# Optimization experiments

Hardware: AMD Instinct MI355X
Metric: run time of the kernel (lower is better)

## Reference

```python
import jax, jax.numpy as jnp
import numpy as np

N = 100000      # num_nodes
E = 3200000     # num_edges (avg degree 32)
DIN, DH, DOUT = 128, 128, 64
S, L = 3, 3     # num_scales, num_layers
EPS = 1e-5


def setup_inputs() -> dict:
    key = jax.random.key(0)
    ks = jax.random.split(key, 12)
    sc = 0.05
    x = jax.random.normal(ks[0], (N, DIN), jnp.float32)
    edge_index = jax.random.randint(ks[1], (2, E), 0, N, jnp.int32)
    return {
        'x': x,
        'edge_index': edge_index,
        'W0': jax.random.normal(ks[2], (S, DIN, DH), jnp.float32) * sc,
        'b0': jnp.zeros((S, DH), jnp.float32),
        'W1': jax.random.normal(ks[3], (S, DH, DH), jnp.float32) * sc,
        'b1': jnp.zeros((S, DH), jnp.float32),
        'W2': jax.random.normal(ks[4], (S, DH, DOUT), jnp.float32) * sc,
        'b2': jnp.zeros((S, DOUT), jnp.float32),
        'gamma': jnp.ones((S * L, DH), jnp.float32),   # layer_norms (only first L-1 per scale used)
        'beta': jnp.zeros((S * L, DH), jnp.float32),
        'Wf': jax.random.normal(ks[5], (S * DOUT, DOUT), jnp.float32) * sc,
        'bf': jnp.zeros((DOUT,), jnp.float32),
    }


def _layer_norm(h, g, b):
    mu = jnp.mean(h, axis=-1, keepdims=True)
    var = jnp.mean(jnp.square(h - mu), axis=-1, keepdims=True)
    return (h - mu) * jax.lax.rsqrt(var + EPS) * g + b


def _gcn(h, W, b, src, dst, dis):
    # GCNConv: D^{-1/2}(A+I)D^{-1/2} h W + b  (self-loops handled separately)
    hw = h @ W
    msg = hw[src] * (dis[src] * dis[dst])[:, None]          # gather + edge-scale
    agg = jax.ops.segment_sum(msg, dst, num_segments=N)     # scatter-add
    agg = agg + hw * (dis * dis)[:, None]                   # self-loop term
    return agg + b


def reference(x, edge_index, W0, b0, W1, b1, W2, b2, gamma, beta, Wf, bf):
    src, dst = edge_index[0], edge_index[1]
    # degree on A + I (unit edge weights + self loop)
    deg = jax.ops.segment_sum(jnp.ones((E,), x.dtype), dst, num_segments=N) + 1.0
    dis = jax.lax.rsqrt(deg)

    scale_outputs = []
    for s in range(S):
        h = _gcn(x, W0[s], b0[s], src, dst, dis)
        h = _layer_norm(jax.nn.relu(h), gamma[s * L + 0], beta[s * L + 0])  # dropout=identity (eval)
        h = _gcn(h, W1[s], b1[s], src, dst, dis)
        h = _layer_norm(jax.nn.relu(h), gamma[s * L + 1], beta[s * L + 1])
        h = _gcn(h, W2[s], b2[s], src, dst, dis)
        scale_outputs.append(h)

    fused = jnp.concatenate(scale_outputs, axis=-1)  # [N, S*DOUT]
    return fused @ Wf + bf
```

## Files before the change

kernel.cpp:

```cpp
#include <hip/hip_runtime.h>

#define DIN 128
#define DH 128
#define DOUTC 64
#define NS 3
#define NL 3
#define EPSV 1e-5f

typedef __attribute__((ext_vector_type(8))) short bf16x8;
typedef __attribute__((ext_vector_type(4))) float f32x4;

static __device__ inline float bf2f(unsigned short h) {
    unsigned int u = ((unsigned int)h) << 16;
    return __builtin_bit_cast(float, u);
}
static __device__ inline unsigned short f2bf(float f) {
    unsigned int u = __builtin_bit_cast(unsigned int, f);
    u += 0x7fffu + ((u >> 16) & 1u);
    return (unsigned short)(u >> 16);
}
static __device__ inline float lo16(unsigned int u) {
    return __builtin_bit_cast(float, u << 16);
}
static __device__ inline float hi16(unsigned int u) {
    return __builtin_bit_cast(float, u & 0xffff0000u);
}
static __device__ inline unsigned int pkbf(float lo, float hi) {
    return ((unsigned int)f2bf(hi) << 16) | f2bf(lo);
}
static __device__ inline float sext8(unsigned int u, int k) {
    return (float)((int)(u << (24 - 8 * k)) >> 24);
}
static __device__ inline unsigned int pk8(float a, float b, float c, float d, float qs) {
    int q0 = (int)rintf(a * qs), q1 = (int)rintf(b * qs);
    int q2 = (int)rintf(c * qs), q3 = (int)rintf(d * qs);
    return (q0 & 255) | ((q1 & 255) << 8) | ((q2 & 255) << 16) | ((q3 & 255) << 24);
}

__global__ __launch_bounds__(256) void k_count_r(const int* __restrict__ dst,
                                                 int* __restrict__ counts, int e, int n) {
    int rg = blockIdx.x & 7;
    int lo = rg * (n >> 3);
    int hi = (rg == 7) ? n : lo + (n >> 3);
    int nb = gridDim.x >> 3, bi = blockIdx.x >> 3;
    int e4 = e >> 2;
    const int4* dst4 = (const int4*)dst;
    for (int i = bi * 256 + threadIdx.x; i < e4; i += nb * 256) {
        int4 d = dst4[i];
        if (d.x >= lo && d.x < hi) atomicAdd(&counts[d.x], 1);
        if (d.y >= lo && d.y < hi) atomicAdd(&counts[d.y], 1);
        if (d.z >= lo && d.z < hi) atomicAdd(&counts[d.z], 1);
        if (d.w >= lo && d.w < hi) atomicAdd(&counts[d.w], 1);
    }
    if (bi == 0 && (int)threadIdx.x < (e & 3)) {
        int d = dst[e4 * 4 + threadIdx.x];
        if (d >= lo && d < hi) atomicAdd(&counts[d], 1);
    }
}

__global__ void k_dis(const int* __restrict__ counts, float* __restrict__ dis, int n) {
    int i = blockIdx.x * blockDim.x + threadIdx.x;
    if (i < n) dis[i] = rsqrtf((float)counts[i] + 1.0f);
}

__global__ void k_scanA(const int* __restrict__ counts, int* __restrict__ row_start,
                        int* __restrict__ bsums, int n) {
    __shared__ int s[512];
    int t = threadIdx.x;
    int i = blockIdx.x * 512 + t;
    int v = (i < n) ? counts[i] : 0;
    s[t] = v;
    __syncthreads();
    for (int off = 1; off < 512; off <<= 1) {
        int x = s[t];
        if (t >= off) x += s[t - off];
        __syncthreads();
        s[t] = x;
        __syncthreads();
    }
    if (i < n) row_start[i] = s[t] - v;
    if (t == 511) bsums[blockIdx.x] = s[511];
}

__global__ void k_scanB(int* __restrict__ bsums, int nb) {
    __shared__ int s[256];
    int t = threadIdx.x;
    int v = (t < nb) ? bsums[t] : 0;
    s[t] = v;
    __syncthreads();
    for (int off = 1; off < 256; off <<= 1) {
        int x = s[t];
        if (t >= off) x += s[t - off];
        __syncthreads();
        s[t] = x;
        __syncthreads();
    }
    if (t < nb) bsums[t] = s[t] - v;
}

__global__ void k_scanC(int* __restrict__ row_start, const int* __restrict__ bsums, int n) {
    int i = blockIdx.x * blockDim.x + threadIdx.x;
    if (i < n) row_start[i] += bsums[i >> 9];
}

__global__ __launch_bounds__(256) void k_fill_r(const int* __restrict__ src,
                                                const int* __restrict__ dst,
                                                int* __restrict__ cursor,
                                                int* __restrict__ col, int e, int n) {
    int rg = blockIdx.x & 7;
    int lo = rg * (n >> 3);
    int hi = (rg == 7) ? n : lo + (n >> 3);
    int nb = gridDim.x >> 3, bi = blockIdx.x >> 3;
    int e4 = e >> 2;
    const int4* dst4 = (const int4*)dst;
    const int4* src4 = (const int4*)src;
    for (int i = bi * 256 + threadIdx.x; i < e4; i += nb * 256) {
        int4 d = dst4[i];
        int4 s = src4[i];
        if (d.x >= lo && d.x < hi) col[atomicAdd(&cursor[d.x], 1)] = s.x;
        if (d.y >= lo && d.y < hi) col[atomicAdd(&cursor[d.y], 1)] = s.y;
        if (d.z >= lo && d.z < hi) col[atomicAdd(&cursor[d.z], 1)] = s.z;
        if (d.w >= lo && d.w < hi) col[atomicAdd(&cursor[d.w], 1)] = s.w;
    }
    if (bi == 0 && (int)threadIdx.x < (e & 3)) {
        int d = dst[e4 * 4 + threadIdx.x];
        int s = src[e4 * 4 + threadIdx.x];
        if (d >= lo && d < hi) col[atomicAdd(&cursor[d], 1)] = s;
    }
}

__global__ void k_prep_w(const float* __restrict__ W0, const float* __restrict__ W1,
                         const float* __restrict__ W2, const float* __restrict__ Wf,
                         const float* __restrict__ b2, const float* __restrict__ bf,
                         unsigned short* __restrict__ Wt0hi, unsigned short* __restrict__ Wt0lo,
                         unsigned short* __restrict__ Wt1hi, unsigned short* __restrict__ Wt1lo,
                         unsigned short* __restrict__ Mhi, unsigned short* __restrict__ Mlo,
                         float* __restrict__ bcomb) {
    int idx = blockIdx.x * blockDim.x + threadIdx.x;
    if (idx < NS * DH * DH) {
        int s = idx / (DH * DH);
        int rem = idx % (DH * DH);
        int o = rem / DH, i = rem % DH;
        {
            float v = W0[(size_t)s * DH * DH + (size_t)i * DH + o];
            unsigned short h = f2bf(v);
            Wt0hi[idx] = h;
            Wt0lo[idx] = f2bf(v - bf2f(h));
        }
        {
            float v = W1[(size_t)s * DH * DH + (size_t)i * DH + o];
            unsigned short h = f2bf(v);
            Wt1hi[idx] = h;
            Wt1lo[idx] = f2bf(v - bf2f(h));
        }
    }
    if (idx < DOUTC * NS * DH) {
        int o = idx / (NS * DH);
        int k = idx % (NS * DH);
        int s = k / DH, i = k % DH;
        float acc = 0.f;
        for (int c = 0; c < DOUTC; ++c)
            acc += W2[((size_t)s * DH + i) * DOUTC + c] * Wf[((size_t)s * DOUTC + c) * DOUTC + o];
        unsigned short h = f2bf(acc);
        Mhi[idx] = h;
        Mlo[idx] = f2bf(acc - bf2f(h));
    }
    if (idx < DOUTC) {
        float acc = bf[idx];
        for (int s = 0; s < NS; ++s)
            for (int c = 0; c < DOUTC; ++c)
                acc += b2[s * DOUTC + c] * Wf[((size_t)s * DOUTC + c) * DOUTC + idx];
        bcomb[idx] = acc;
    }
}

__global__ __launch_bounds__(256) void k_cvtq(const float2* __restrict__ x,
                                              unsigned int* __restrict__ xq,
                                              float* __restrict__ xs,
                                              const float* __restrict__ dis, int n) {
    int wid = ((blockIdx.x * blockDim.x + threadIdx.x) >> 6);
    int lane = threadIdx.x & 63;
    if (wid >= n) return;
    float2 v = x[(size_t)wid * 64 + lane];
    float m = fmaxf(fabsf(v.x), fabsf(v.y));
    #pragma unroll
    for (int off = 32; off; off >>= 1) m = fmaxf(m, __shfl_xor(m, off));
    float qs = m > 0.f ? 127.f / m : 0.f;
    int q0 = (int)rintf(v.x * qs), q1 = (int)rintf(v.y * qs);
    ((unsigned short*)xq)[(size_t)wid * 64 + lane] =
        (unsigned short)((q0 & 255) | ((q1 & 255) << 8));
    if (lane == 0) xs[wid] = dis[wid] * m * (1.f / 127.f);
}

__global__ __launch_bounds__(256) void k_quant384(const unsigned int* __restrict__ h,
                                                  unsigned int* __restrict__ hq,
                                                  float* __restrict__ hs, int n) {
    int wid = ((blockIdx.x * blockDim.x + threadIdx.x) >> 6);
    int lane = threadIdx.x & 63;
    int half = lane >> 5, c = lane & 31;
    int v = wid * 2 + half;
    if (v >= n) return;
    const uint2* p = (const uint2*)(h + (size_t)v * 192);
    uint2 w0 = p[c], w1 = p[c + 32], w2 = p[c + 64];
    float f[12] = {lo16(w0.x), hi16(w0.x), lo16(w0.y), hi16(w0.y),
                   lo16(w1.x), hi16(w1.x), lo16(w1.y), hi16(w1.y),
                   lo16(w2.x), hi16(w2.x), lo16(w2.y), hi16(w2.y)};
    float m = 0.f;
    #pragma unroll
    for (int k = 0; k < 12; ++k) m = fmaxf(m, fabsf(f[k]));
    #pragma unroll
    for (int off = 16; off; off >>= 1) m = fmaxf(m, __shfl_xor(m, off));
    float qs = m > 0.f ? 127.f / m : 0.f;
    unsigned int* po = hq + (size_t)v * 96;
    po[c]      = pk8(f[0], f[1], f[2], f[3], qs);
    po[c + 32] = pk8(f[4], f[5], f[6], f[7], qs);
    po[c + 64] = pk8(f[8], f[9], f[10], f[11], qs);
    if (c == 0) hs[v] = m * (1.f / 127.f);
}

__global__ __launch_bounds__(256) void k_quant64(const unsigned int* __restrict__ qb,
                                                 unsigned int* __restrict__ qq,
                                                 float* __restrict__ qs2, int n) {
    int wid = ((blockIdx.x * blockDim.x + threadIdx.x) >> 6);
    int lane = threadIdx.x & 63;
    int g = lane >> 4, c = lane & 15;
    int v = wid * 4 + g;
    if (v >= n) return;
    uint2 w = ((const uint2*)(qb + (size_t)v * 32))[c];
    float f0 = lo16(w.x), f1 = hi16(w.x), f2 = lo16(w.y), f3 = hi16(w.y);
    float m = fmaxf(fmaxf(fabsf(f0), fabsf(f1)), fmaxf(fabsf(f2), fabsf(f3)));
    #pragma unroll
    for (int off = 8; off; off >>= 1) m = fmaxf(m, __shfl_xor(m, off));
    float qs = m > 0.f ? 127.f / m : 0.f;
    qq[(size_t)v * 16 + c] = pk8(f0, f1, f2, f3, qs);
    if (c == 0) qs2[v] = m * (1.f / 127.f);
}

__global__ __launch_bounds__(256) void k_agg128q(
        const unsigned int* __restrict__ xq, const float* __restrict__ xs,
        unsigned int* __restrict__ z0, const float* __restrict__ dis,
        const int* __restrict__ rowstart, const int* __restrict__ counts,
        const int* __restrict__ col, int n) {
    int wid = (blockIdx.x * blockDim.x + threadIdx.x) >> 6;
    int lane = threadIdx.x & 63;
    int half = lane >> 5, c = lane & 31;
    int nw = (gridDim.x * blockDim.x) >> 6;
    int ntask = (n + 1) >> 1;
    for (int w = wid; w < ntask; w += nw) {
        int v = w * 2 + half;
        int vc = v < n ? v : n - 1;
        float dv = dis[vc];
        const int* colp = col + rowstart[vc];
        int cnt = v < n ? counts[vc] : 0;
        unsigned int us = xq[(size_t)vc * 32 + c];
        float sv = xs[vc];
        float a0 = sv * sext8(us, 0), a1 = sv * sext8(us, 1);
        float a2 = sv * sext8(us, 2), a3 = sv * sext8(us, 3);
        int i = 0;
        for (; i + 8 <= cnt; i += 8) {
            #pragma unroll
            for (int k = 0; k < 8; ++k) {
                int s0 = colp[i + k];
                float sc = xs[s0];
                unsigned int u = xq[(size_t)s0 * 32 + c];
                a0 += sc * sext8(u, 0); a1 += sc * sext8(u, 1);
                a2 += sc * sext8(u, 2); a3 += sc * sext8(u, 3);
            }
        }
        for (; i < cnt; ++i) {
            int s0 = colp[i];
            float sc = xs[s0];
            unsigned int u = xq[(size_t)s0 * 32 + c];
            a0 += sc * sext8(u, 0); a1 += sc * sext8(u, 1);
            a2 += sc * sext8(u, 2); a3 += sc * sext8(u, 3);
        }
        if (v < n) {
            uint2 o = {pkbf(dv * a0, dv * a1), pkbf(dv * a2, dv * a3)};
            *(uint2*)&z0[(size_t)v * 64 + 2 * c] = o;
        }
    }
}

__global__ __launch_bounds__(256) void k_agg384q(
        const unsigned int* __restrict__ hq, const float* __restrict__ hs,
        unsigned int* __restrict__ g1, const float* __restrict__ dis,
        const int* __restrict__ rowstart, const int* __restrict__ counts,
        const int* __restrict__ col, int n) {
    int wid = (blockIdx.x * blockDim.x + threadIdx.x) >> 6;
    int lane = threadIdx.x & 63;
    int half = lane >> 5, c = lane & 31;
    int nw = (gridDim.x * blockDim.x) >> 6;
    int ntask = (n + 1) >> 1;
    for (int w = wid; w < ntask; w += nw) {
        int v = w * 2 + half;
        int vc = v < n ? v : n - 1;
        float dv = dis[vc];
        const int* colp = col + rowstart[vc];
        int cnt = v < n ? counts[vc] : 0;
        const unsigned int* rp = hq + (size_t)vc * 96;
        unsigned int u0 = rp[c], u1 = rp[c + 32], u2 = rp[c + 64];
        float sv = hs[vc];
        float a[12];
        #pragma unroll
        for (int k = 0; k < 4; ++k) {
            a[k]     = sv * sext8(u0, k);
            a[4 + k] = sv * sext8(u1, k);
            a[8 + k] = sv * sext8(u2, k);
        }
        int i = 0;
        for (; i + 4 <= cnt; i += 4) {
            #pragma unroll
            for (int k4 = 0; k4 < 4; ++k4) {
                int s0 = colp[i + k4];
                float sc = hs[s0];
                const unsigned int* p0 = hq + (size_t)s0 * 96;
                unsigned int w0 = p0[c], w1 = p0[c + 32], w2 = p0[c + 64];
                #pragma unroll
                for (int k = 0; k < 4; ++k) {
                    a[k]     += sc * sext8(w0, k);
                    a[4 + k] += sc * sext8(w1, k);
                    a[8 + k] += sc * sext8(w2, k);
                }
            }
        }
        for (; i < cnt; ++i) {
            int s0 = colp[i];
            float sc = hs[s0];
            const unsigned int* p0 = hq + (size_t)s0 * 96;
            unsigned int w0 = p0[c], w1 = p0[c + 32], w2 = p0[c + 64];
            #pragma unroll
            for (int k = 0; k < 4; ++k) {
                a[k]     += sc * sext8(w0, k);
                a[4 + k] += sc * sext8(w1, k);
                a[8 + k] += sc * sext8(w2, k);
            }
        }
        if (v < n) {
            unsigned int* po = g1 + (size_t)v * 192;
            uint2 o0 = {pkbf(dv * a[0], dv * a[1]), pkbf(dv * a[2], dv * a[3])};
            *(uint2*)&po[2 * c] = o0;
            uint2 o1 = {pkbf(dv * a[4], dv * a[5]), pkbf(dv * a[6], dv * a[7])};
            *(uint2*)&po[2 * c + 64] = o1;
            uint2 o2 = {pkbf(dv * a[8], dv * a[9]), pkbf(dv * a[10], dv * a[11])};
            *(uint2*)&po[2 * c + 128] = o2;
        }
    }
}

__global__ __launch_bounds__(256) void k_agg64q(
        const unsigned int* __restrict__ qq, const float* __restrict__ qs2,
        float* __restrict__ out, const float* __restrict__ bcomb,
        const float* __restrict__ dis, const int* __restrict__ rowstart,
        const int* __restrict__ counts, const int* __restrict__ col, int n) {
    int wid = (blockIdx.x * blockDim.x + threadIdx.x) >> 6;
    int lane = threadIdx.x & 63;
    int g = lane >> 4, c = lane & 15;
    int nw = (gridDim.x * blockDim.x) >> 6;
    int ntask = (n + 3) >> 2;
    float4 bc = ((const float4*)bcomb)[c];
    for (int w = wid; w < ntask; w += nw) {
        int v = w * 4 + g;
        int vc = v < n ? v : n - 1;
        float dv = dis[vc];
        const int* colp = col + rowstart[vc];
        int cnt = v < n ? counts[vc] : 0;
        unsigned int us = qq[(size_t)vc * 16 + c];
        float sv = qs2[vc];
        float a0 = sv * sext8(us, 0), a1 = sv * sext8(us, 1);
        float a2 = sv * sext8(us, 2), a3 = sv * sext8(us, 3);
        int i = 0;
        for (; i + 8 <= cnt; i += 8) {
            #pragma unroll
            for (int k = 0; k < 8; ++k) {
                int s0 = colp[i + k];
                float sc = qs2[s0];
                unsigned int u = qq[(size_t)s0 * 16 + c];
                a0 += sc * sext8(u, 0); a1 += sc * sext8(u, 1);
                a2 += sc * sext8(u, 2); a3 += sc * sext8(u, 3);
            }
        }
        for (; i < cnt; ++i) {
            int s0 = colp[i];
            float sc = qs2[s0];
            unsigned int u = qq[(size_t)s0 * 16 + c];
            a0 += sc * sext8(u, 0); a1 += sc * sext8(u, 1);
            a2 += sc * sext8(u, 2); a3 += sc * sext8(u, 3);
        }
        if (v < n) {
            float4 o = make_float4(dv * a0 + bc.x, dv * a1 + bc.y,
                                   dv * a2 + bc.z, dv * a3 + bc.w);
            *(float4*)&out[(size_t)v * 64 + 4 * c] = o;
        }
    }
}

__global__ __launch_bounds__(256) void k_gemm0(
        const unsigned short* __restrict__ A, const unsigned short* __restrict__ Whi,
        const unsigned short* __restrict__ Wlo, const float* __restrict__ bias,
        const float* __restrict__ gamma, const float* __restrict__ beta,
        const float* __restrict__ dis, unsigned short* __restrict__ out, int n) {
    int wave = threadIdx.x >> 6, lane = threadIdx.x & 63;
    int g = blockIdx.x * 4 + wave;
    if (g * 16 >= n) return;
    int r16 = lane & 15, g4 = lane >> 4;
    int row = g * 16 + r16;
    if (row >= n) row = n - 1;

    bf16x8 a[4];
    #pragma unroll
    for (int ks = 0; ks < 4; ++ks)
        a[ks] = *(const bf16x8*)&A[(size_t)row * DH + ks * 32 + g4 * 8];

    for (int s = 0; s < NS; ++s) {
        const unsigned short* whi = Whi + (size_t)s * DH * DH;
        const unsigned short* wlo = Wlo + (size_t)s * DH * DH;
        f32x4 acc[8];
        #pragma unroll
        for (int t = 0; t < 8; ++t) acc[t] = (f32x4){0.f, 0.f, 0.f, 0.f};
        #pragma unroll
        for (int ks = 0; ks < 4; ++ks) {
            #pragma unroll
            for (int t = 0; t < 8; ++t) {
                size_t wofs = (size_t)(t * 16 + r16) * DH + ks * 32 + g4 * 8;
                bf16x8 bh = *(const bf16x8*)&whi[wofs];
                bf16x8 bl = *(const bf16x8*)&wlo[wofs];
                acc[t] = __builtin_amdgcn_mfma_f32_16x16x32_bf16(a[ks], bh, acc[t], 0, 0, 0);
                acc[t] = __builtin_amdgcn_mfma_f32_16x16x32_bf16(a[ks], bl, acc[t], 0, 0, 0);
            }
        }
        float bia[8], gam[8], bet[8];
        #pragma unroll
        for (int t = 0; t < 8; ++t) {
            bia[t] = bias[s * DH + t * 16 + r16];
            gam[t] = gamma[(size_t)(s * NL + 0) * DH + t * 16 + r16];
            bet[t] = beta[(size_t)(s * NL + 0) * DH + t * 16 + r16];
        }
        #pragma unroll
        for (int r = 0; r < 4; ++r) {
            float y[8];
            float sm = 0.f, q = 0.f;
            #pragma unroll
            for (int t = 0; t < 8; ++t) {
                y[t] = fmaxf(acc[t][r] + bia[t], 0.f);
                sm += y[t];
                q += y[t] * y[t];
            }
            #pragma unroll
            for (int off = 8; off; off >>= 1) {
                sm += __shfl_xor(sm, off);
                q += __shfl_xor(q, off);
            }
            float mu = sm * (1.f / 128.f);
            float var = q * (1.f / 128.f) - mu * mu;
            float rstd = rsqrtf(var + EPSV);
            int node = g * 16 + g4 * 4 + r;
            if (node < n) {
                float dnode = dis[node];
                #pragma unroll
                for (int t = 0; t < 8; ++t) {
                    float o = ((y[t] - mu) * rstd * gam[t] + bet[t]) * dnode;
                    out[(size_t)node * (NS * DH) + s * DH + t * 16 + r16] = f2bf(o);
                }
            }
        }
    }
}

__global__ __launch_bounds__(256) void k_gemm1q(
        const unsigned short* __restrict__ G, const unsigned short* __restrict__ Whi,
        const unsigned short* __restrict__ Wlo, const unsigned short* __restrict__ Mhi,
        const unsigned short* __restrict__ Mlo, const float* __restrict__ bias,
        const float* __restrict__ gamma, const float* __restrict__ beta,
        const float* __restrict__ dis, unsigned short* __restrict__ q, int n) {
    __shared__ __align__(16) unsigned short sH[4][16][392];
    int wave = threadIdx.x >> 6, lane = threadIdx.x & 63;
    int g = blockIdx.x * 4 + wave;
    if (g * 16 >= n) return;
    int r16 = lane & 15, g4 = lane >> 4;
    int row = g * 16 + r16;
    if (row >= n) row = n - 1;

    for (int s = 0; s < NS; ++s) {
        bf16x8 a[4];
        #pragma unroll
        for (int ks = 0; ks < 4; ++ks)
            a[ks] = *(const bf16x8*)&G[(size_t)row * (NS * DH) + s * DH + ks * 32 + g4 * 8];
        const unsigned short* whi = Whi + (size_t)s * DH * DH;
        const unsigned short* wlo = Wlo + (size_t)s * DH * DH;
        f32x4 acc[8];
        #pragma unroll
        for (int t = 0; t < 8; ++t) acc[t] = (f32x4){0.f, 0.f, 0.f, 0.f};
        #pragma unroll
        for (int ks = 0; ks < 4; ++ks) {
            #pragma unroll
            for (int t = 0; t < 8; ++t) {
                size_t wofs = (size_t)(t * 16 + r16) * DH + ks * 32 + g4 * 8;
                bf16x8 bh = *(const bf16x8*)&whi[wofs];
                bf16x8 bl = *(const bf16x8*)&wlo[wofs];
                acc[t] = __builtin_amdgcn_mfma_f32_16x16x32_bf16(a[ks], bh, acc[t], 0, 0, 0);
                acc[t] = __builtin_amdgcn_mfma_f32_16x16x32_bf16(a[ks], bl, acc[t], 0, 0, 0);
            }
        }
        float bia[8], gam[8], bet[8];
        #pragma unroll
        for (int t = 0; t < 8; ++t) {
            bia[t] = bias[s * DH + t * 16 + r16];
            gam[t] = gamma[(size_t)(s * NL + 1) * DH + t * 16 + r16];
            bet[t] = beta[(size_t)(s * NL + 1) * DH + t * 16 + r16];
        }
        #pragma unroll
        for (int r = 0; r < 4; ++r) {
            float y[8];
            float sm = 0.f, qq = 0.f;
            #pragma unroll
            for (int t = 0; t < 8; ++t) {
                y[t] = fmaxf(acc[t][r] + bia[t], 0.f);
                sm += y[t];
                qq += y[t] * y[t];
            }
            #pragma unroll
            for (int off = 8; off; off >>= 1) {
                sm += __shfl_xor(sm, off);
                qq += __shfl_xor(qq, off);
            }
            float mu = sm * (1.f / 128.f);
            float var = qq * (1.f / 128.f) - mu * mu;
            float rstd = rsqrtf(var + EPSV);
            #pragma unroll
            for (int t = 0; t < 8; ++t) {
                float o = (y[t] - mu) * rstd * gam[t] + bet[t];
                sH[wave][g4 * 4 + r][s * DH + t * 16 + r16] = f2bf(o);
            }
        }
    }
    __syncthreads();
    f32x4 qa[4];
    #pragma unroll
    for (int t = 0; t < 4; ++t) qa[t] = (f32x4){0.f, 0.f, 0.f, 0.f};
    #pragma unroll
    for (int ks = 0; ks < 12; ++ks) {
        bf16x8 av = *(const bf16x8*)&sH[wave][r16][ks * 32 + g4 * 8];
        #pragma unroll
        for (int t = 0; t < 4; ++t) {
            size_t wofs = (size_t)(t * 16 + r16) * (NS * DH) + ks * 32 + g4 * 8;
            bf16x8 bh = *(const bf16x8*)&Mhi[wofs];
            bf16x8 bl = *(const bf16x8*)&Mlo[wofs];
            qa[t] = __builtin_amdgcn_mfma_f32_16x16x32_bf16(av, bh, qa[t], 0, 0, 0);
            qa[t] = __builtin_amdgcn_mfma_f32_16x16x32_bf16(av, bl, qa[t], 0, 0, 0);
        }
    }
    #pragma unroll
    for (int r = 0; r < 4; ++r) {
        int node = g * 16 + g4 * 4 + r;
        if (node < n) {
            float dnode = dis[node];
            #pragma unroll
            for (int t = 0; t < 4; ++t)
                q[(size_t)node * DOUTC + t * 16 + r16] = f2bf(qa[t][r] * dnode);
        }
    }
}

extern "C" void kernel_launch(void* const* d_in, const int* in_sizes, int n_in,
                              void* d_out, int out_size, void* d_ws, size_t ws_size,
                              hipStream_t stream) {
    const float* x    = (const float*)d_in[0];
    const int*   ei   = (const int*)d_in[1];
    const float* W0   = (const float*)d_in[2];
    const float* b0   = (const float*)d_in[3];
    const float* W1   = (const float*)d_in[4];
    const float* b1   = (const float*)d_in[5];
    const float* W2   = (const float*)d_in[6];
    const float* b2   = (const float*)d_in[7];
    const float* gamma= (const float*)d_in[8];
    const float* beta = (const float*)d_in[9];
    const float* Wf   = (const float*)d_in[10];
    const float* bf   = (const float*)d_in[11];
    float* out = (float*)d_out;

    const int n = in_sizes[0] / DIN;
    const int e = in_sizes[1] / 2;
    const int* src = ei;
    const int* dst = ei + e;

    char* ws = (char*)d_ws;
    auto alloc = [&](size_t bytes) {
        char* p = ws;
        ws += (bytes + 255) & ~(size_t)255;
        return p;
    };
    int*   counts   = (int*)alloc((size_t)n * 4);
    int*   cursor   = (int*)alloc((size_t)n * 4);
    int*   rowstart = (int*)alloc((size_t)n * 4);
    int*   bsums    = (int*)alloc(4096);
    float* dis      = (float*)alloc((size_t)n * 4);
    int*   col      = (int*)alloc((size_t)e * 4);
    unsigned short* Wt0hi = (unsigned short*)alloc((size_t)NS * DH * DH * 2);
    unsigned short* Wt0lo = (unsigned short*)alloc((size_t)NS * DH * DH * 2);
    unsigned short* Wt1hi = (unsigned short*)alloc((size_t)NS * DH * DH * 2);
    unsigned short* Wt1lo = (unsigned short*)alloc((size_t)NS * DH * DH * 2);
    unsigned short* Mhi   = (unsigned short*)alloc((size_t)DOUTC * NS * DH * 2);
    unsigned short* Mlo   = (unsigned short*)alloc((size_t)DOUTC * NS * DH * 2);
    float* bcomb    = (float*)alloc(DOUTC * 4);
    unsigned int* xq  = (unsigned int*)alloc((size_t)n * 32 * 4);
    float* xs         = (float*)alloc((size_t)n * 4);
    unsigned short* z0    = (unsigned short*)alloc((size_t)n * DH * 2);
    unsigned short* h1cat = (unsigned short*)alloc((size_t)n * NS * DH * 2);
    unsigned int* h1q = (unsigned int*)alloc((size_t)n * 96 * 4);
    float* hs         = (float*)alloc((size_t)n * 4);
    unsigned short* g1cat = (unsigned short*)alloc((size_t)n * NS * DH * 2);
    unsigned short* q     = (unsigned short*)alloc((size_t)n * DOUTC * 2);
    unsigned int* qq  = (unsigned int*)alloc((size_t)n * 16 * 4);
    float* qs2        = (float*)alloc((size_t)n * 4);

    hipMemsetAsync(counts, 0, (size_t)n * 4, stream);

    k_count_r<<<2048, 256, 0, stream>>>(dst, counts, e, n);
    k_dis<<<(n + 255) / 256, 256, 0, stream>>>(counts, dis, n);

    int nb = (n + 511) / 512;
    k_scanA<<<nb, 512, 0, stream>>>(counts, rowstart, bsums, n);
    k_scanB<<<1, 256, 0, stream>>>(bsums, nb);
    k_scanC<<<(n + 255) / 256, 256, 0, stream>>>(rowstart, bsums, n);
    hipMemcpyAsync(cursor, rowstart, (size_t)n * 4, hipMemcpyDeviceToDevice, stream);
    k_fill_r<<<2048, 256, 0, stream>>>(src, dst, cursor, col, e, n);

    k_prep_w<<<(NS * DH * DH + 255) / 256, 256, 0, stream>>>(
        W0, W1, W2, Wf, b2, bf, Wt0hi, Wt0lo, Wt1hi, Wt1lo, Mhi, Mlo, bcomb);
    k_cvtq<<<(n + 3) / 4, 256, 0, stream>>>((const float2*)x, xq, xs, dis, n);

    k_agg128q<<<2048, 256, 0, stream>>>(xq, xs, (unsigned int*)z0,
                                        dis, rowstart, counts, col, n);
    const int GG = (n / 16 + 3) / 4;
    k_gemm0<<<GG, 256, 0, stream>>>(z0, Wt0hi, Wt0lo, b0, gamma, beta, dis, h1cat, n);
    k_quant384<<<(n + 7) / 8, 256, 0, stream>>>((const unsigned int*)h1cat, h1q, hs, n);
    k_agg384q<<<2048, 256, 0, stream>>>(h1q, hs, (unsigned int*)g1cat,
                                        dis, rowstart, counts, col, n);
    k_gemm1q<<<GG, 256, 0, stream>>>(g1cat, Wt1hi, Wt1lo, Mhi, Mlo,
                                     b1, gamma, beta, dis, q, n);
    k_quant64<<<(n + 15) / 16, 256, 0, stream>>>((const unsigned int*)q, qq, qs2, n);
    k_agg64q<<<2048, 256, 0, stream>>>(qq, qs2, out, bcomb,
                                       dis, rowstart, counts, col, n);
}
```

Before: 1.242 ms.

## Fuse int8 quantization into GEMM epilogues with permuted channel layout

Layer-0 GEMM now quantizes its LayerNorm output straight to int8 with a per-scale scale factor, removing the separate quant384 kernel and the bf16 h1cat round trip. Channels are stored in a permuted order so each lane writes contiguous packed words, and W1 and the fused W2·Wf matrix are permuted to match. The second GEMM is split into k_gemm1, which writes bf16 h2, and k_gemmq, which does the final projection and quantizes inline, replacing gemm1q's shared-memory staging and the quant64 kernel. The trade-off is an extra global write and read of h2 and three per-scale quantization scales instead of one.

```diff
diff --git a/kernel.cpp b/kernel.cpp
--- a/kernel.cpp
+++ b/kernel.cpp
@@ -148,7 +148,10 @@
             Wt0lo[idx] = f2bf(v - bf2f(h));
         }
         {
-            float v = W1[(size_t)s * DH * DH + (size_t)i * DH + o];
+            int lp = i;
+            int p = lp >> 6, r = (lp >> 2) & 15, k = lp & 3;
+            int lchan = (4 * p + k) * 16 + r;
+            float v = W1[(size_t)s * DH * DH + (size_t)lchan * DH + o];
             unsigned short h = f2bf(v);
             Wt1hi[idx] = h;
             Wt1lo[idx] = f2bf(v - bf2f(h));
@@ -156,11 +159,13 @@
     }
     if (idx < DOUTC * NS * DH) {
         int o = idx / (NS * DH);
-        int k = idx % (NS * DH);
-        int s = k / DH, i = k % DH;
+        int pos = idx % (NS * DH);
+        int s = pos >> 7, lp = pos & 127;
+        int p = lp >> 6, r = (lp >> 2) & 15, k = lp & 3;
+        int il = (4 * p + k) * 16 + r;
         float acc = 0.f;
         for (int c = 0; c < DOUTC; ++c)
-            acc += W2[((size_t)s * DH + i) * DOUTC + c] * Wf[((size_t)s * DOUTC + c) * DOUTC + o];
+            acc += W2[((size_t)s * DH + il) * DOUTC + c] * Wf[((size_t)s * DOUTC + c) * DOUTC + o];
         unsigned short h = f2bf(acc);
         Mhi[idx] = h;
         Mlo[idx] = f2bf(acc - bf2f(h));
@@ -190,50 +195,6 @@
     ((unsigned short*)xq)[(size_t)wid * 64 + lane] =
         (unsigned short)((q0 & 255) | ((q1 & 255) << 8));
     if (lane == 0) xs[wid] = dis[wid] * m * (1.f / 127.f);
-}
-
-__global__ __launch_bounds__(256) void k_quant384(const unsigned int* __restrict__ h,
-                                                  unsigned int* __restrict__ hq,
-                                                  float* __restrict__ hs, int n) {
-    int wid = ((blockIdx.x * blockDim.x + threadIdx.x) >> 6);
-    int lane = threadIdx.x & 63;
-    int half = lane >> 5, c = lane & 31;
-    int v = wid * 2 + half;
-    if (v >= n) return;
-    const uint2* p = (const uint2*)(h + (size_t)v * 192);
-    uint2 w0 = p[c], w1 = p[c + 32], w2 = p[c + 64];
-    float f[12] = {lo16(w0.x), hi16(w0.x), lo16(w0.y), hi16(w0.y),
-                   lo16(w1.x), hi16(w1.x), lo16(w1.y), hi16(w1.y),
-                   lo16(w2.x), hi16(w2.x), lo16(w2.y), hi16(w2.y)};
-    float m = 0.f;
-    #pragma unroll
-    for (int k = 0; k < 12; ++k) m = fmaxf(m, fabsf(f[k]));
-    #pragma unroll
-    for (int off = 16; off; off >>= 1) m = fmaxf(m, __shfl_xor(m, off));
-    float qs = m > 0.f ? 127.f / m : 0.f;
-    unsigned int* po = hq + (size_t)v * 96;
-    po[c]      = pk8(f[0], f[1], f[2], f[3], qs);
-    po[c + 32] = pk8(f[4], f[5], f[6], f[7], qs);
-    po[c + 64] = pk8(f[8], f[9], f[10], f[11], qs);
-    if (c == 0) hs[v] = m * (1.f / 127.f);
-}
-
-__global__ __launch_bounds__(256) void k_quant64(const unsigned int* __restrict__ qb,
-                                                 unsigned int* __restrict__ qq,
-                                                 float* __restrict__ qs2, int n) {
-    int wid = ((blockIdx.x * blockDim.x + threadIdx.x) >> 6);
-    int lane = threadIdx.x & 63;
-    int g = lane >> 4, c = lane & 15;
-    int v = wid * 4 + g;
-    if (v >= n) return;
-    uint2 w = ((const uint2*)(qb + (size_t)v * 32))[c];
-    float f0 = lo16(w.x), f1 = hi16(w.x), f2 = lo16(w.y), f3 = hi16(w.y);
-    float m = fmaxf(fmaxf(fabsf(f0), fabsf(f1)), fmaxf(fabsf(f2), fabsf(f3)));
-    #pragma unroll
-    for (int off = 8; off; off >>= 1) m = fmaxf(m, __shfl_xor(m, off));
-    float qs = m > 0.f ? 127.f / m : 0.f;
-    qq[(size_t)v * 16 + c] = pk8(f0, f1, f2, f3, qs);
-    if (c == 0) qs2[v] = m * (1.f / 127.f);
 }
 
 __global__ __launch_bounds__(256) void k_agg128q(
@@ -281,8 +242,89 @@
     }
 }
 
-__global__ __launch_bounds__(256) void k_agg384q(
-        const unsigned int* __restrict__ hq, const float* __restrict__ hs,
+__global__ __launch_bounds__(256, 4) void k_gemm0i(
+        const unsigned short* __restrict__ A, const unsigned short* __restrict__ Whi,
+        const unsigned short* __restrict__ Wlo, const float* __restrict__ bias,
+        const float* __restrict__ gamma, const float* __restrict__ beta,
+        const float* __restrict__ dis, unsigned int* __restrict__ h1q,
+        float* __restrict__ hs4, int n) {
+    int wave = threadIdx.x >> 6, lane = threadIdx.x & 63;
+    int g = blockIdx.x * 4 + wave;
+    if (g * 16 >= n) return;
+    int r16 = lane & 15, g4 = lane >> 4;
+    int row = g * 16 + r16;
+    if (row >= n) row = n - 1;
+
+    bf16x8 a[4];
+    #pragma unroll
+    for (int ks = 0; ks < 4; ++ks)
+        a[ks] = *(const bf16x8*)&A[(size_t)row * DH + ks * 32 + g4 * 8];
+
+    for (int s = 0; s < NS; ++s) {
+        const unsigned short* whi = Whi + (size_t)s * DH * DH;
+        const unsigned short* wlo = Wlo + (size_t)s * DH * DH;
+        f32x4 acc[8];
+        #pragma unroll
+        for (int t = 0; t < 8; ++t) acc[t] = (f32x4){0.f, 0.f, 0.f, 0.f};
+        #pragma unroll
+        for (int ks = 0; ks < 4; ++ks) {
+            #pragma unroll
+            for (int t = 0; t < 8; ++t) {
+                size_t wofs = (size_t)(t * 16 + r16) * DH + ks * 32 + g4 * 8;
+                bf16x8 bh = *(const bf16x8*)&whi[wofs];
+                bf16x8 bl = *(const bf16x8*)&wlo[wofs];
+                acc[t] = __builtin_amdgcn_mfma_f32_16x16x32_bf16(a[ks], bh, acc[t], 0, 0, 0);
+                acc[t] = __builtin_amdgcn_mfma_f32_16x16x32_bf16(a[ks], bl, acc[t], 0, 0, 0);
+            }
+        }
+        float bia[8], gam[8], bet[8];
+        #pragma unroll
+        for (int t = 0; t < 8; ++t) {
+            bia[t] = bias[s * DH + t * 16 + r16];
+            gam[t] = gamma[(size_t)(s * NL + 0) * DH + t * 16 + r16];
+            bet[t] = beta[(size_t)(s * NL + 0) * DH + t * 16 + r16];
+        }
+        #pragma unroll
+        for (int r = 0; r < 4; ++r) {
+            float y[8];
+            float sm = 0.f, q = 0.f;
+            #pragma unroll
+            for (int t = 0; t < 8; ++t) {
+                y[t] = fmaxf(acc[t][r] + bia[t], 0.f);
+                sm += y[t];
+                q += y[t] * y[t];
+            }
+            #pragma unroll
+            for (int off = 8; off; off >>= 1) {
+                sm += __shfl_xor(sm, off);
+                q += __shfl_xor(q, off);
+            }
+            float mu = sm * (1.f / 128.f);
+            float var = q * (1.f / 128.f) - mu * mu;
+            float rstd = rsqrtf(var + EPSV);
+            float o[8];
+            float m = 0.f;
+            #pragma unroll
+            for (int t = 0; t < 8; ++t) {
+                o[t] = (y[t] - mu) * rstd * gam[t] + bet[t];
+                m = fmaxf(m, fabsf(o[t]));
+            }
+            #pragma unroll
+            for (int off = 8; off; off >>= 1) m = fmaxf(m, __shfl_xor(m, off));
+            float qs = m > 0.f ? 127.f / m : 0.f;
+            int node = g * 16 + g4 * 4 + r;
+            if (node < n) {
+                unsigned int* pn = h1q + (size_t)node * 96;
+                pn[(s * 2 + 0) * 16 + r16] = pk8(o[0], o[1], o[2], o[3], qs);
+                pn[(s * 2 + 1) * 16 + r16] = pk8(o[4], o[5], o[6], o[7], qs);
+                if (r16 == 0) hs4[(size_t)node * 4 + s] = dis[node] * m * (1.f / 127.f);
+            }
+        }
+    }
+}
+
+__global__ __launch_bounds__(256) void k_agg384qp(
+        const unsigned int* __restrict__ hq, const float* __restrict__ hs4,
         unsigned int* __restrict__ g1, const float* __restrict__ dis,
         const int* __restrict__ rowstart, const int* __restrict__ counts,
         const int* __restrict__ col, int n) {
@@ -299,50 +341,166 @@
         int cnt = v < n ? counts[vc] : 0;
         const unsigned int* rp = hq + (size_t)vc * 96;
         unsigned int u0 = rp[c], u1 = rp[c + 32], u2 = rp[c + 64];
-        float sv = hs[vc];
+        float4 sv = ((const float4*)hs4)[vc];
         float a[12];
         #pragma unroll
         for (int k = 0; k < 4; ++k) {
-            a[k]     = sv * sext8(u0, k);
-            a[4 + k] = sv * sext8(u1, k);
-            a[8 + k] = sv * sext8(u2, k);
+            a[k]     = sv.x * sext8(u0, k);
+            a[4 + k] = sv.y * sext8(u1, k);
+            a[8 + k] = sv.z * sext8(u2, k);
         }
         int i = 0;
         for (; i + 4 <= cnt; i += 4) {
             #pragma unroll
             for (int k4 = 0; k4 < 4; ++k4) {
                 int s0 = colp[i + k4];
-                float sc = hs[s0];
+                float4 sc = ((const float4*)hs4)[s0];
                 const unsigned int* p0 = hq + (size_t)s0 * 96;
                 unsigned int w0 = p0[c], w1 = p0[c + 32], w2 = p0[c + 64];
                 #pragma unroll
                 for (int k = 0; k < 4; ++k) {
-                    a[k]     += sc * sext8(w0, k);
-                    a[4 + k] += sc * sext8(w1, k);
-                    a[8 + k] += sc * sext8(w2, k);
+                    a[k]     += sc.x * sext8(w0, k);
+                    a[4 + k] += sc.y * sext8(w1, k);
+                    a[8 + k] += sc.z * sext8(w2, k);
                 }
             }
         }
         for (; i < cnt; ++i) {
             int s0 = colp[i];
-            float sc = hs[s0];
+            float4 sc = ((const float4*)hs4)[s0];
             const unsigned int* p0 = hq + (size_t)s0 * 96;
             unsigned int w0 = p0[c], w1 = p0[c + 32], w2 = p0[c + 64];
             #pragma unroll
             for (int k = 0; k < 4; ++k) {
-                a[k]     += sc * sext8(w0, k);
-                a[4 + k] += sc * sext8(w1, k);
-                a[8 + k] += sc * sext8(w2, k);
+                a[k]     += sc.x * sext8(w0, k);
+                a[4 + k] += sc.y * sext8(w1, k);
+                a[8 + k] += sc.z * sext8(w2, k);
             }
         }
         if (v < n) {
             unsigned int* po = g1 + (size_t)v * 192;
+            int b = ((c >> 4) & 1) * 32 + (c & 15) * 2;
             uint2 o0 = {pkbf(dv * a[0], dv * a[1]), pkbf(dv * a[2], dv * a[3])};
-            *(uint2*)&po[2 * c] = o0;
+            *(uint2*)&po[b] = o0;
             uint2 o1 = {pkbf(dv * a[4], dv * a[5]), pkbf(dv * a[6], dv * a[7])};
-            *(uint2*)&po[2 * c + 64] = o1;
+            *(uint2*)&po[b + 64] = o1;
             uint2 o2 = {pkbf(dv * a[8], dv * a[9]), pkbf(dv * a[10], dv * a[11])};
-            *(uint2*)&po[2 * c + 128] = o2;
+            *(uint2*)&po[b + 128] = o2;
+        }
+    }
+}
+
+__global__ __launch_bounds__(256, 4) void k_gemm1(
+        const unsigned short* __restrict__ G, const unsigned short* __restrict__ Whi,
+        const unsigned short* __restrict__ Wlo, const float* __restrict__ bias,
+        const float* __restrict__ gamma, const float* __restrict__ beta,
+        unsigned int* __restrict__ h2, int n) {
+    int wave = threadIdx.x >> 6, lane = threadIdx.x & 63;
+    int g = blockIdx.x * 4 + wave;
+    if (g * 16 >= n) return;
+    int r16 = lane & 15, g4 = lane >> 4;
+    int row = g * 16 + r16;
+    if (row >= n) row = n - 1;
+
+    for (int s = 0; s < NS; ++s) {
+        bf16x8 a[4];
+        #pragma unroll
+        for (int ks = 0; ks < 4; ++ks)
+            a[ks] = *(const bf16x8*)&G[(size_t)row * (NS * DH) + s * DH + ks * 32 + g4 * 8];
+        const unsigned short* whi = Whi + (size_t)s * DH * DH;
+        const unsigned short* wlo = Wlo + (size_t)s * DH * DH;
+        f32x4 acc[8];
+        #pragma unroll
+        for (int t = 0; t < 8; ++t) acc[t] = (f32x4){0.f, 0.f, 0.f, 0.f};
+        #pragma unroll
+        for (int ks = 0; ks < 4; ++ks) {
+            #pragma unroll
+            for (int t = 0; t < 8; ++t) {
+                size_t wofs = (size_t)(t * 16 + r16) * DH + ks * 32 + g4 * 8;
+                bf16x8 bh = *(const bf16x8*)&whi[wofs];
+                bf16x8 bl = *(const bf16x8*)&wlo[wofs];
+                acc[t] = __builtin_amdgcn_mfma_f32_16x16x32_bf16(a[ks], bh, acc[t], 0, 0, 0);
+                acc[t] = __builtin_amdgcn_mfma_f32_16x16x32_bf16(a[ks], bl, acc[t], 0, 0, 0);
+            }
+        }
+        float bia[8], gam[8], bet[8];
+        #pragma unroll
+        for (int t = 0; t < 8; ++t) {
+            bia[t] = bias[s * DH + t * 16 + r16];
+            gam[t] = gamma[(size_t)(s * NL + 1) * DH + t * 16 + r16];
+            bet[t] = beta[(size_t)(s * NL + 1) * DH + t * 16 + r16];
+        }
+        #pragma unroll
+        for (int r = 0; r < 4; ++r) {
+            float y[8];
+            float sm = 0.f, qq = 0.f;
+            #pragma unroll
+            for (int t = 0; t < 8; ++t) {
+                y[t] = fmaxf(acc[t][r] + bia[t], 0.f);
+                sm += y[t];
+                qq += y[t] * y[t];
+            }
+            #pragma unroll
+            for (int off = 8; off; off >>= 1) {
+                sm += __shfl_xor(sm, off);
+                qq += __shfl_xor(qq, off);
+            }
+            float mu = sm * (1.f / 128.f);
+            float var = qq * (1.f / 128.f) - mu * mu;
+            float rstd = rsqrtf(var + EPSV);
+            float o[8];
+            #pragma unroll
+            for (int t = 0; t < 8; ++t)
+                o[t] = (y[t] - mu) * rstd * gam[t] + bet[t];
+            int node = g * 16 + g4 * 4 + r;
+            if (node < n) {
+                unsigned int* po = h2 + (size_t)node * 192;
+                uint2 w0 = {pkbf(o[0], o[1]), pkbf(o[2], o[3])};
+                *(uint2*)&po[s * 64 + r16 * 2] = w0;
+                uint2 w1 = {pkbf(o[4], o[5]), pkbf(o[6], o[7])};
+                *(uint2*)&po[s * 64 + 32 + r16 * 2] = w1;
+            }
+        }
+    }
+}
+
+__global__ __launch_bounds__(256, 4) void k_gemmq(
+        const unsigned short* __restrict__ H, const unsigned short* __restrict__ Mhi,
+        const unsigned short* __restrict__ Mlo, const float* __restrict__ dis,
+        unsigned int* __restrict__ qq, float* __restrict__ qs2, int n) {
+    int wave = threadIdx.x >> 6, lane = threadIdx.x & 63;
+    int g = blockIdx.x * 4 + wave;
+    if (g * 16 >= n) return;
+    int r16 = lane & 15, g4 = lane >> 4;
+    int row = g * 16 + r16;
+    if (row >= n) row = n - 1;
+
+    f32x4 qa[4];
+    #pragma unroll
+    for (int t = 0; t < 4; ++t) qa[t] = (f32x4){0.f, 0.f, 0.f, 0.f};
+    #pragma unroll
+    for (int ks = 0; ks < 12; ++ks) {
+        bf16x8 av = *(const bf16x8*)&H[(size_t)row * (NS * DH) + ks * 32 + g4 * 8];
+        #pragma unroll
+        for (int t = 0; t < 4; ++t) {
+            size_t wofs = (size_t)(t * 16 + r16) * (NS * DH) + ks * 32 + g4 * 8;
+            bf16x8 bh = *(const bf16x8*)&Mhi[wofs];
+            bf16x8 bl = *(const bf16x8*)&Mlo[wofs];
+            qa[t] = __builtin_amdgcn_mfma_f32_16x16x32_bf16(av, bh, qa[t], 0, 0, 0);
+            qa[t] = __builtin_amdgcn_mfma_f32_16x16x32_bf16(av, bl, qa[t], 0, 0, 0);
+        }
+    }
+    #pragma unroll
+    for (int r = 0; r < 4; ++r) {
+        float v0 = qa[0][r], v1 = qa[1][r], v2 = qa[2][r], v3 = qa[3][r];
+        float m = fmaxf(fmaxf(fabsf(v0), fabsf(v1)), fmaxf(fabsf(v2), fabsf(v3)));
+        #pragma unroll
+        for (int off = 8; off; off >>= 1) m = fmaxf(m, __shfl_xor(m, off));
+        float qs = m > 0.f ? 127.f / m : 0.f;
+        int node = g * 16 + g4 * 4 + r;
+        if (node < n) {
+            qq[(size_t)node * 16 + r16] = pk8(v0, v1, v2, v3, qs);
+            if (r16 == 0) qs2[node] = dis[node] * m * (1.f / 127.f);
         }
     }
 }
@@ -357,7 +515,7 @@
     int g = lane >> 4, c = lane & 15;
     int nw = (gridDim.x * blockDim.x) >> 6;
     int ntask = (n + 3) >> 2;
-    float4 bc = ((const float4*)bcomb)[c];
+    float bc0 = bcomb[c], bc1 = bcomb[16 + c], bc2 = bcomb[32 + c], bc3 = bcomb[48 + c];
     for (int w = wid; w < ntask; w += nw) {
         int v = w * 4 + g;
         int vc = v < n ? v : n - 1;
@@ -387,176 +545,11 @@
             a2 += sc * sext8(u, 2); a3 += sc * sext8(u, 3);
         }
         if (v < n) {
-            float4 o = make_float4(dv * a0 + bc.x, dv * a1 + bc.y,
-                                   dv * a2 + bc.z, dv * a3 + bc.w);
-            *(float4*)&out[(size_t)v * 64 + 4 * c] = o;
-        }
-    }
-}
-
-__global__ __launch_bounds__(256) void k_gemm0(
-        const unsigned short* __restrict__ A, const unsigned short* __restrict__ Whi,
-        const unsigned short* __restrict__ Wlo, const float* __restrict__ bias,
-        const float* __restrict__ gamma, const float* __restrict__ beta,
-        const float* __restrict__ dis, unsigned short* __restrict__ out, int n) {
-    int wave = threadIdx.x >> 6, lane = threadIdx.x & 63;
-    int g = blockIdx.x * 4 + wave;
-    if (g * 16 >= n) return;
-    int r16 = lane & 15, g4 = lane >> 4;
-    int row = g * 16 + r16;
-    if (row >= n) row = n - 1;
-
-    bf16x8 a[4];
-    #pragma unroll
-    for (int ks = 0; ks < 4; ++ks)
-        a[ks] = *(const bf16x8*)&A[(size_t)row * DH + ks * 32 + g4 * 8];
-
-    for (int s = 0; s < NS; ++s) {
-        const unsigned short* whi = Whi + (size_t)s * DH * DH;
-        const unsigned short* wlo = Wlo + (size_t)s * DH * DH;
-        f32x4 acc[8];
-        #pragma unroll
-        for (int t = 0; t < 8; ++t) acc[t] = (f32x4){0.f, 0.f, 0.f, 0.f};
-        #pragma unroll
-        for (int ks = 0; ks < 4; ++ks) {
-            #pragma unroll
-            for (int t = 0; t < 8; ++t) {
-                size_t wofs = (size_t)(t * 16 + r16) * DH + ks * 32 + g4 * 8;
-                bf16x8 bh = *(const bf16x8*)&whi[wofs];
-                bf16x8 bl = *(const bf16x8*)&wlo[wofs];
-                acc[t] = __builtin_amdgcn_mfma_f32_16x16x32_bf16(a[ks], bh, acc[t], 0, 0, 0);
-                acc[t] = __builtin_amdgcn_mfma_f32_16x16x32_bf16(a[ks], bl, acc[t], 0, 0, 0);
-            }
-        }
-        float bia[8], gam[8], bet[8];
-        #pragma unroll
-        for (int t = 0; t < 8; ++t) {
-            bia[t] = bias[s * DH + t * 16 + r16];
-            gam[t] = gamma[(size_t)(s * NL + 0) * DH + t * 16 + r16];
-            bet[t] = beta[(size_t)(s * NL + 0) * DH + t * 16 + r16];
-        }
-        #pragma unroll
-        for (int r = 0; r < 4; ++r) {
-            float y[8];
-            float sm = 0.f, q = 0.f;
-            #pragma unroll
-            for (int t = 0; t < 8; ++t) {
-                y[t] = fmaxf(acc[t][r] + bia[t], 0.f);
-                sm += y[t];
-                q += y[t] * y[t];
-            }
-            #pragma unroll
-            for (int off = 8; off; off >>= 1) {
-                sm += __shfl_xor(sm, off);
-                q += __shfl_xor(q, off);
-            }
-            float mu = sm * (1.f / 128.f);
-            float var = q * (1.f / 128.f) - mu * mu;
-            float rstd = rsqrtf(var + EPSV);
-            int node = g * 16 + g4 * 4 + r;
-            if (node < n) {
-                float dnode = dis[node];
-                #pragma unroll
-                for (int t = 0; t < 8; ++t) {
-                    float o = ((y[t] - mu) * rstd * gam[t] + bet[t]) * dnode;
-                    out[(size_t)node * (NS * DH) + s * DH + t * 16 + r16] = f2bf(o);
-                }
-            }
-        }
-    }
-}
-
-__global__ __launch_bounds__(256) void k_gemm1q(
-        const unsigned short* __restrict__ G, const unsigned short* __restrict__ Whi,
-        const unsigned short* __restrict__ Wlo, const unsigned short* __restrict__ Mhi,
-        const unsigned short* __restrict__ Mlo, const float* __restrict__ bias,
-        const float* __restrict__ gamma, const float* __restrict__ beta,
-        const float* __restrict__ dis, unsigned short* __restrict__ q, int n) {
-    __shared__ __align__(16) unsigned short sH[4][16][392];
-    int wave = threadIdx.x >> 6, lane = threadIdx.x & 63;
-    int g = blockIdx.x * 4 + wave;
-    if (g * 16 >= n) return;
-    int r16 = lane & 15, g4 = lane >> 4;
-    int row = g * 16 + r16;
-    if (row >= n) row = n - 1;
-
-    for (int s = 0; s < NS; ++s) {
-        bf16x8 a[4];
-        #pragma unroll
-        for (int ks = 0; ks < 4; ++ks)
-            a[ks] = *(const bf16x8*)&G[(size_t)row * (NS * DH) + s * DH + ks * 32 + g4 * 8];
-        const unsigned short* whi = Whi + (size_t)s * DH * DH;
-        const unsigned short* wlo = Wlo + (size_t)s * DH * DH;
-        f32x4 acc[8];
-        #pragma unroll
-        for (int t = 0; t < 8; ++t) acc[t] = (f32x4){0.f, 0.f, 0.f, 0.f};
-        #pragma unroll
-        for (int ks = 0; ks < 4; ++ks) {
-            #pragma unroll
-            for (int t = 0; t < 8; ++t) {
-                size_t wofs = (size_t)(t * 16 + r16) * DH + ks * 32 + g4 * 8;
-                bf16x8 bh = *(const bf16x8*)&whi[wofs];
-                bf16x8 bl = *(const bf16x8*)&wlo[wofs];
-                acc[t] = __builtin_amdgcn_mfma_f32_16x16x32_bf16(a[ks], bh, acc[t], 0, 0, 0);
-                acc[t] = __builtin_amdgcn_mfma_f32_16x16x32_bf16(a[ks], bl, acc[t], 0, 0, 0);
-            }
-        }
-        float bia[8], gam[8], bet[8];
-        #pragma unroll
-        for (int t = 0; t < 8; ++t) {
-            bia[t] = bias[s * DH + t * 16 + r16];
-            gam[t] = gamma[(size_t)(s * NL + 1) * DH + t * 16 + r16];
-            bet[t] = beta[(size_t)(s * NL + 1) * DH + t * 16 + r16];
-        }
-        #pragma unroll
-        for (int r = 0; r < 4; ++r) {
-            float y[8];
-            float sm = 0.f, qq = 0.f;
-            #pragma unroll
-            for (int t = 0; t < 8; ++t) {
-                y[t] = fmaxf(acc[t][r] + bia[t], 0.f);
-                sm += y[t];
-                qq += y[t] * y[t];
-            }
-            #pragma unroll
-            for (int off = 8; off; off >>= 1) {
-                sm += __shfl_xor(sm, off);
-                qq += __shfl_xor(qq, off);
-            }
-            float mu = sm * (1.f / 128.f);
-            float var = qq * (1.f / 128.f) - mu * mu;
-            float rstd = rsqrtf(var + EPSV);
-            #pragma unroll
-            for (int t = 0; t < 8; ++t) {
-                float o = (y[t] - mu) * rstd * gam[t] + bet[t];
-                sH[wave][g4 * 4 + r][s * DH + t * 16 + r16] = f2bf(o);
-            }
-        }
-    }
-    __syncthreads();
-    f32x4 qa[4];
-    #pragma unroll
-    for (int t = 0; t < 4; ++t) qa[t] = (f32x4){0.f, 0.f, 0.f, 0.f};
-    #pragma unroll
-    for (int ks = 0; ks < 12; ++ks) {
-        bf16x8 av = *(const bf16x8*)&sH[wave][r16][ks * 32 + g4 * 8];
-        #pragma unroll
-        for (int t = 0; t < 4; ++t) {
-            size_t wofs = (size_t)(t * 16 + r16) * (NS * DH) + ks * 32 + g4 * 8;
-            bf16x8 bh = *(const bf16x8*)&Mhi[wofs];
-            bf16x8 bl = *(const bf16x8*)&Mlo[wofs];
-            qa[t] = __builtin_amdgcn_mfma_f32_16x16x32_bf16(av, bh, qa[t], 0, 0, 0);
-            qa[t] = __builtin_amdgcn_mfma_f32_16x16x32_bf16(av, bl, qa[t], 0, 0, 0);
-        }
-    }
-    #pragma unroll
-    for (int r = 0; r < 4; ++r) {
-        int node = g * 16 + g4 * 4 + r;
-        if (node < n) {
-            float dnode = dis[node];
-            #pragma unroll
-            for (int t = 0; t < 4; ++t)
-                q[(size_t)node * DOUTC + t * 16 + r16] = f2bf(qa[t][r] * dnode);
+            float* po = out + (size_t)v * 64;
+            po[c]      = dv * a0 + bc0;
+            po[16 + c] = dv * a1 + bc1;
+            po[32 + c] = dv * a2 + bc2;
+            po[48 + c] = dv * a3 + bc3;
         }
     }
 }
@@ -604,12 +597,11 @@
     float* bcomb    = (float*)alloc(DOUTC * 4);
     unsigned int* xq  = (unsigned int*)alloc((size_t)n * 32 * 4);
     float* xs         = (float*)alloc((size_t)n * 4);
-    unsigned short* z0    = (unsigned short*)alloc((size_t)n * DH * 2);
-    unsigned short* h1cat = (unsigned short*)alloc((size_t)n * NS * DH * 2);
+    unsigned short* z0 = (unsigned short*)alloc((size_t)n * DH * 2);
     unsigned int* h1q = (unsigned int*)alloc((size_t)n * 96 * 4);
-    float* hs         = (float*)alloc((size_t)n * 4);
+    float* hs4        = (float*)alloc((size_t)n * 16);
     unsigned short* g1cat = (unsigned short*)alloc((size_t)n * NS * DH * 2);
-    unsigned short* q     = (unsigned short*)alloc((size_t)n * DOUTC * 2);
+    unsigned int* h2  = (unsigned int*)alloc((size_t)n * 192 * 4);
     unsigned int* qq  = (unsigned int*)alloc((size_t)n * 16 * 4);
     float* qs2        = (float*)alloc((size_t)n * 4);
 
@@ -632,13 +624,11 @@
     k_agg128q<<<2048, 256, 0, stream>>>(xq, xs, (unsigned int*)z0,
                                         dis, rowstart, counts, col, n);
     const int GG = (n / 16 + 3) / 4;
-    k_gemm0<<<GG, 256, 0, stream>>>(z0, Wt0hi, Wt0lo, b0, gamma, beta, dis, h1cat, n);
-    k_quant384<<<(n + 7) / 8, 256, 0, stream>>>((const unsigned int*)h1cat, h1q, hs, n);
-    k_agg384q<<<2048, 256, 0, stream>>>(h1q, hs, (unsigned int*)g1cat,
-                                        dis, rowstart, counts, col, n);
-    k_gemm1q<<<GG, 256, 0, stream>>>(g1cat, Wt1hi, Wt1lo, Mhi, Mlo,
-                                     b1, gamma, beta, dis, q, n);
-    k_quant64<<<(n + 15) / 16, 256, 0, stream>>>((const unsigned int*)q, qq, qs2, n);
+    k_gemm0i<<<GG, 256, 0, stream>>>(z0, Wt0hi, Wt0lo, b0, gamma, beta, dis, h1q, hs4, n);
+    k_agg384qp<<<2048, 256, 0, stream>>>(h1q, hs4, (unsigned int*)g1cat,
+                                         dis, rowstart, counts, col, n);
+    k_gemm1<<<GG, 256, 0, stream>>>(g1cat, Wt1hi, Wt1lo, b1, gamma, beta, h2, n);
+    k_gemmq<<<GG, 256, 0, stream>>>((const unsigned short*)h2, Mhi, Mlo, dis, qq, qs2, n);
     k_agg64q<<<2048, 256, 0, stream>>>(qq, qs2, out, bcomb,
                                        dis, rowstart, counts, col, n);
 }
```

Result: slower. 1.367 ms (+10.1%).
